# Optimization experiments

Hardware: AMD Instinct MI355X
Metric: run time of the kernel (lower is better)

The kernel has to match this reference:

```python
import jax, jax.numpy as jnp
import numpy as np

N = 50000   # nodes (cells)
E = 800000  # directed edges
D = 512     # input/output feature dim (genes)
H = D // 64 # bottleneck dim = 8
LN_EPS = 1e-5


def setup_inputs() -> dict:
    key = jax.random.key(0)
    ks = jax.random.split(key, 6)
    x = jax.random.normal(ks[0], (N, D), dtype=jnp.float32)
    edge_index = jax.random.randint(ks[1], (2, E), 0, N, dtype=jnp.int64)
    size_factors = jax.random.uniform(ks[2], (N, 1), dtype=jnp.float32) + 0.5
    s1 = float(1.0 / np.sqrt(D))
    W1 = jax.random.uniform(ks[3], (D, H), jnp.float32, -s1, s1)
    b1 = jnp.zeros((H,), jnp.float32)
    gamma = jnp.ones((H,), jnp.float32)
    beta = jnp.zeros((H,), jnp.float32)
    s2 = float(1.0 / np.sqrt(H))
    W2 = jax.random.uniform(ks[4], (H, D), jnp.float32, -s2, s2)
    b2 = jnp.zeros((D,), jnp.float32)
    return {"x": x, "size_factors": size_factors, "W1": W1, "b1": b1,
            "gamma": gamma, "beta": beta, "W2": W2, "b2": b2,
            "edge_index": edge_index}


def _gcn_conv(x, W, b, src, dst, norm):
    # PyG GCNConv: linear transform, then sym-normalized scatter-add aggregation.
    h = x @ W                                   # [N, out]
    msg = h[src] * norm[:, None]                # [E+N, out] gather + scale
    out = jax.ops.segment_sum(msg, dst, num_segments=N)  # scatter-add
    return out + b


def reference(x, size_factors, W1, b1, gamma, beta, W2, b2, edge_index):
    loops = jnp.arange(N, dtype=edge_index.dtype)
    src = jnp.concatenate([edge_index[0], loops])  # add self-loops
    dst = jnp.concatenate([edge_index[1], loops])
    deg = jax.ops.segment_sum(jnp.ones_like(src, dtype=x.dtype), dst,
                              num_segments=N)       # deg >= 1 via self-loops
    dinv = jax.lax.rsqrt(deg)
    norm = dinv[src] * dinv[dst]                    # [E+N]

    h = _gcn_conv(x, W1, b1, src, dst, norm)        # [N, H]
    mu = jnp.mean(h, axis=-1, keepdims=True)
    var = jnp.var(h, axis=-1, keepdims=True)
    h = (h - mu) * jax.lax.rsqrt(var + LN_EPS) * gamma + beta
    h = jax.nn.relu(h)
    # dropout p=0.0 -> identity
    out = jax.nn.relu(_gcn_conv(h, W2, b2, src, dst, norm))  # [N, D]
    return out * size_factors
```

## Files before the change

### kernel.cpp

```cpp
#include <hip/hip_runtime.h>

#define NN 50000
#define EE 800000
#define DD 512
#define HH 8
#define SLOTS 64
#define NBLK 196
#define NTILE (NN/16)
#define EBLK (EE/256)

typedef short bf16x8 __attribute__((ext_vector_type(8)));
typedef float f32x4 __attribute__((ext_vector_type(4)));

union U16 { uint4 u; bf16x8 v; unsigned short h[8]; };

__device__ __forceinline__ unsigned short f2bf(float f) {
    union { float f; unsigned int i; } c; c.f = f;
    unsigned int i = c.i;
    i += 0x7fffu + ((i >> 16) & 1u);
    return (unsigned short)(i >> 16);
}

__global__ void k_fill_ell(const int* __restrict__ src, const int* __restrict__ dst,
                           int* __restrict__ cur, int* __restrict__ slots) {
    int e = blockIdx.x * 256 + threadIdx.x;
    if (e >= EE) return;
    int s = src[e], d = dst[e];
    int pos = atomicAdd(&cur[d], 1);
    if (pos < SLOTS) slots[(size_t)pos * NN + d] = s;
}

__global__ __launch_bounds__(256) void k_gemm1(const float4* __restrict__ x4,
                                               const float* __restrict__ W1,
                                               float* __restrict__ t1) {
    __shared__ unsigned short sbf[16 * 64 * 8];
    for (int i = threadIdx.x; i < 16 * 64 * 8; i += 256) {
        int lane = (i >> 3) & 63, j = i & 7;
        int n = lane & 15;
        int k = (i >> 9) * 32 + ((lane >> 4) * 8) + j;
        sbf[i] = (n < HH) ? f2bf(W1[k * HH + n]) : (unsigned short)0;
    }
    __syncthreads();
    int wave = threadIdx.x >> 6, lane = threadIdx.x & 63;
    int tile = blockIdx.x * 4 + wave;
    if (tile >= NTILE) return;
    int node0 = tile * 16;
    int m = lane & 15, q = lane >> 4;
    const float4* xrow = x4 + (size_t)(node0 + m) * (DD / 4) + q * 2;
    const uint4* bfrag = (const uint4*)sbf;
    f32x4 acc = {0.f, 0.f, 0.f, 0.f};
#pragma unroll
    for (int step = 0; step < 16; ++step) {
        float4 u0 = xrow[step * 8];
        float4 u1 = xrow[step * 8 + 1];
        U16 a, b;
        a.h[0] = f2bf(u0.x); a.h[1] = f2bf(u0.y); a.h[2] = f2bf(u0.z); a.h[3] = f2bf(u0.w);
        a.h[4] = f2bf(u1.x); a.h[5] = f2bf(u1.y); a.h[6] = f2bf(u1.z); a.h[7] = f2bf(u1.w);
        b.u = bfrag[step * 64 + lane];
        acc = __builtin_amdgcn_mfma_f32_16x16x32_bf16(a.v, b.v, acc, 0, 0, 0);
    }
    if (m < HH) {
        int base = (node0 + q * 4) * HH + m;
        t1[base]          = acc[0];
        t1[base + HH]     = acc[1];
        t1[base + 2 * HH] = acc[2];
        t1[base + 3 * HH] = acc[3];
    }
}

__global__ void k_agg1(const float4* __restrict__ t1v, const int* __restrict__ cur,
                       const int* __restrict__ slots,
                       const float* __restrict__ b1,
                       const float* __restrict__ gma,
                       const float* __restrict__ bta,
                       float4* __restrict__ h2v) {
    int n = blockIdx.x * 256 + threadIdx.x;
    if (n >= NN) return;
    int deg = cur[n]; if (deg > SLOTS) deg = SLOTS;
    float dv = rsqrtf((float)cur[n] + 1.0f);
    float4 p0 = t1v[2 * n], p1 = t1v[2 * n + 1];
    float a0 = p0.x * dv, a1 = p0.y * dv, a2 = p0.z * dv, a3 = p0.w * dv;
    float a4 = p1.x * dv, a5 = p1.y * dv, a6 = p1.z * dv, a7 = p1.w * dv;
    for (int i = 0; i < deg; ++i) {
        int s = slots[(size_t)i * NN + n];
        float ws = rsqrtf((float)cur[s] + 1.0f);
        float4 q0 = t1v[2 * s], q1 = t1v[2 * s + 1];
        a0 += q0.x * ws; a1 += q0.y * ws; a2 += q0.z * ws; a3 += q0.w * ws;
        a4 += q1.x * ws; a5 += q1.y * ws; a6 += q1.z * ws; a7 += q1.w * ws;
    }
    a0 = a0 * dv + b1[0]; a1 = a1 * dv + b1[1]; a2 = a2 * dv + b1[2]; a3 = a3 * dv + b1[3];
    a4 = a4 * dv + b1[4]; a5 = a5 * dv + b1[5]; a6 = a6 * dv + b1[6]; a7 = a7 * dv + b1[7];
    float mu = (a0 + a1 + a2 + a3 + a4 + a5 + a6 + a7) * 0.125f;
    float d0 = a0 - mu, d1 = a1 - mu, d2 = a2 - mu, d3 = a3 - mu;
    float d4 = a4 - mu, d5 = a5 - mu, d6 = a6 - mu, d7 = a7 - mu;
    float var = (d0*d0 + d1*d1 + d2*d2 + d3*d3 + d4*d4 + d5*d5 + d6*d6 + d7*d7) * 0.125f;
    float rs = rsqrtf(var + 1e-5f);
    float r0 = fmaxf(d0 * rs * gma[0] + bta[0], 0.f);
    float r1 = fmaxf(d1 * rs * gma[1] + bta[1], 0.f);
    float r2 = fmaxf(d2 * rs * gma[2] + bta[2], 0.f);
    float r3 = fmaxf(d3 * rs * gma[3] + bta[3], 0.f);
    float r4 = fmaxf(d4 * rs * gma[4] + bta[4], 0.f);
    float r5 = fmaxf(d5 * rs * gma[5] + bta[5], 0.f);
    float r6 = fmaxf(d6 * rs * gma[6] + bta[6], 0.f);
    float r7 = fmaxf(d7 * rs * gma[7] + bta[7], 0.f);
    h2v[2 * n]     = make_float4(r0, r1, r2, r3);
    h2v[2 * n + 1] = make_float4(r4, r5, r6, r7);
}

__global__ void k_agg2(const float4* __restrict__ h2v, const int* __restrict__ cur,
                       const int* __restrict__ slots, float4* __restrict__ aggv) {
    int n = blockIdx.x * 256 + threadIdx.x;
    if (n >= NN) return;
    int deg = cur[n]; if (deg > SLOTS) deg = SLOTS;
    float dv = rsqrtf((float)cur[n] + 1.0f);
    float4 p0 = h2v[2 * n], p1 = h2v[2 * n + 1];
    float a0 = p0.x * dv, a1 = p0.y * dv, a2 = p0.z * dv, a3 = p0.w * dv;
    float a4 = p1.x * dv, a5 = p1.y * dv, a6 = p1.z * dv, a7 = p1.w * dv;
    for (int i = 0; i < deg; ++i) {
        int s = slots[(size_t)i * NN + n];
        float ws = rsqrtf((float)cur[s] + 1.0f);
        float4 q0 = h2v[2 * s], q1 = h2v[2 * s + 1];
        a0 += q0.x * ws; a1 += q0.y * ws; a2 += q0.z * ws; a3 += q0.w * ws;
        a4 += q1.x * ws; a5 += q1.y * ws; a6 += q1.z * ws; a7 += q1.w * ws;
    }
    aggv[2 * n]     = make_float4(a0 * dv, a1 * dv, a2 * dv, a3 * dv);
    aggv[2 * n + 1] = make_float4(a4 * dv, a5 * dv, a6 * dv, a7 * dv);
}

__global__ __launch_bounds__(256) void k_gemm2(const float4* __restrict__ aggv,
                                               const float* __restrict__ W2,
                                               const float* __restrict__ b2,
                                               const float* __restrict__ sf,
                                               float* __restrict__ out) {
    int c = threadIdx.x & 63;
    int g = threadIdx.x >> 6;
    int d0 = c * 8;
    float w[8][8];
#pragma unroll
    for (int k = 0; k < 8; ++k) {
        float4 u0 = *(const float4*)(W2 + k * DD + d0);
        float4 u1 = *(const float4*)(W2 + k * DD + d0 + 4);
        w[k][0] = u0.x; w[k][1] = u0.y; w[k][2] = u0.z; w[k][3] = u0.w;
        w[k][4] = u1.x; w[k][5] = u1.y; w[k][6] = u1.z; w[k][7] = u1.w;
    }
    float bb[8];
    {
        float4 u0 = *(const float4*)(b2 + d0);
        float4 u1 = *(const float4*)(b2 + d0 + 4);
        bb[0] = u0.x; bb[1] = u0.y; bb[2] = u0.z; bb[3] = u0.w;
        bb[4] = u1.x; bb[5] = u1.y; bb[6] = u1.z; bb[7] = u1.w;
    }
#pragma unroll
    for (int i = 0; i < 8; ++i) {
        int n = blockIdx.x * 32 + i * 4 + g;
        if (n < NN) {
            float4 p0 = aggv[2 * n], p1 = aggv[2 * n + 1];
            float a[8] = {p0.x, p0.y, p0.z, p0.w, p1.x, p1.y, p1.z, p1.w};
            float s = sf[n];
            float acc[8];
#pragma unroll
            for (int j = 0; j < 8; ++j) acc[j] = bb[j];
#pragma unroll
            for (int k = 0; k < 8; ++k)
#pragma unroll
                for (int j = 0; j < 8; ++j) acc[j] += a[k] * w[k][j];
            float4 o0 = make_float4(fmaxf(acc[0], 0.f) * s, fmaxf(acc[1], 0.f) * s,
                                    fmaxf(acc[2], 0.f) * s, fmaxf(acc[3], 0.f) * s);
            float4 o1 = make_float4(fmaxf(acc[4], 0.f) * s, fmaxf(acc[5], 0.f) * s,
                                    fmaxf(acc[6], 0.f) * s, fmaxf(acc[7], 0.f) * s);
            float4* op = (float4*)(out + (size_t)n * DD + d0);
            op[0] = o0;
            op[1] = o1;
        }
    }
}

extern "C" void kernel_launch(void* const* d_in, const int* in_sizes, int n_in,
                              void* d_out, int out_size, void* d_ws, size_t ws_size,
                              hipStream_t stream) {
    (void)in_sizes; (void)n_in; (void)out_size; (void)ws_size;
    const float* x   = (const float*)d_in[0];
    const float* sf  = (const float*)d_in[1];
    const float* W1  = (const float*)d_in[2];
    const float* b1  = (const float*)d_in[3];
    const float* gma = (const float*)d_in[4];
    const float* bta = (const float*)d_in[5];
    const float* W2  = (const float*)d_in[6];
    const float* b2  = (const float*)d_in[7];
    const int* eidx  = (const int*)d_in[8];
    float* out = (float*)d_out;

    char* ws = (char*)d_ws;
    int*   cur   = (int*)(ws + 0);
    int*   slots = (int*)(ws + (1 << 20));
    float* t1    = (float*)(ws + 15 * (1 << 20));
    float* h2    = (float*)(ws + 17 * (1 << 20));
    float* agg2  = (float*)(ws + 19 * (1 << 20));

    hipMemsetAsync(cur, 0, NN * sizeof(int), stream);
    k_fill_ell<<<EBLK, 256, 0, stream>>>(eidx, eidx + EE, cur, slots);
    k_gemm1<<<(NTILE + 3) / 4, 256, 0, stream>>>((const float4*)x, W1, t1);
    k_agg1<<<NBLK, 256, 0, stream>>>((const float4*)t1, cur, slots,
                                     b1, gma, bta, (float4*)h2);
    k_agg2<<<NBLK, 256, 0, stream>>>((const float4*)h2, cur, slots,
                                     (float4*)agg2);
    k_gemm2<<<(NN + 31) / 32, 256, 0, stream>>>((const float4*)agg2, W2, b2, sf, out);
}
```

Measured before the change: 303.6 us.

## Fuse ELL fill with GEMM1, fuse agg2 with GEMM2, parallelize aggregation per feature

Merges the edge-to-ELL fill and the first GEMM into one launch by giving each its own range of block indices. The second aggregation is fused into the output GEMM through shared memory, which removes the agg2 intermediate buffer and one launch. Both aggregations now use 8 threads per node, one per feature, instead of one thread per node. This is meant to raise parallelism and occupancy on the latency-bound gathers, and LayerNorm is computed with shuffles across those 8 threads. In exchange each gathered row is read with more, smaller loads, and the gather loop is unrolled by two with a ballot-based exit.

```diff
diff --git a/kernel.cpp b/kernel.cpp
--- a/kernel.cpp
+++ b/kernel.cpp
@@ -5,9 +5,10 @@
 #define DD 512
 #define HH 8
 #define SLOTS 64
-#define NBLK 196
-#define NTILE (NN/16)
-#define EBLK (EE/256)
+#define GBLK 782
+#define EBLK 3125
+#define NTILE 3125
+#define AGBLK 1563
 
 typedef short bf16x8 __attribute__((ext_vector_type(8)));
 typedef float f32x4 __attribute__((ext_vector_type(4)));
@@ -21,18 +22,21 @@
     return (unsigned short)(i >> 16);
 }
 
-__global__ void k_fill_ell(const int* __restrict__ src, const int* __restrict__ dst,
-                           int* __restrict__ cur, int* __restrict__ slots) {
-    int e = blockIdx.x * 256 + threadIdx.x;
-    if (e >= EE) return;
-    int s = src[e], d = dst[e];
-    int pos = atomicAdd(&cur[d], 1);
-    if (pos < SLOTS) slots[(size_t)pos * NN + d] = s;
-}
-
-__global__ __launch_bounds__(256) void k_gemm1(const float4* __restrict__ x4,
-                                               const float* __restrict__ W1,
-                                               float* __restrict__ t1) {
+__global__ __launch_bounds__(256) void k_fill_gemm1(const int* __restrict__ eidx,
+                                                    const float4* __restrict__ x4,
+                                                    const float* __restrict__ W1,
+                                                    int* __restrict__ cur,
+                                                    int* __restrict__ slots,
+                                                    float* __restrict__ t1) {
+    if (blockIdx.x >= GBLK) {
+        int e = (blockIdx.x - GBLK) * 256 + threadIdx.x;
+        if (e < EE) {
+            int s = eidx[e], d = eidx[EE + e];
+            int pos = atomicAdd(&cur[d], 1);
+            if (pos < SLOTS) slots[(size_t)pos * NN + d] = s;
+        }
+        return;
+    }
     __shared__ unsigned short sbf[16 * 64 * 8];
     for (int i = threadIdx.x; i < 16 * 64 * 8; i += 256) {
         int lane = (i >> 3) & 63, j = i & 7;
@@ -68,73 +72,54 @@
     }
 }
 
-__global__ void k_agg1(const float4* __restrict__ t1v, const int* __restrict__ cur,
-                       const int* __restrict__ slots,
-                       const float* __restrict__ b1,
-                       const float* __restrict__ gma,
-                       const float* __restrict__ bta,
-                       float4* __restrict__ h2v) {
-    int n = blockIdx.x * 256 + threadIdx.x;
+__global__ __launch_bounds__(256) void k_agg1(const float* __restrict__ t1,
+                                              const int* __restrict__ cur,
+                                              const int* __restrict__ slots,
+                                              const float* __restrict__ b1,
+                                              const float* __restrict__ gma,
+                                              const float* __restrict__ bta,
+                                              float* __restrict__ h2) {
+    int gid = blockIdx.x * 256 + threadIdx.x;
+    int n = gid >> 3, f = gid & 7;
     if (n >= NN) return;
-    int deg = cur[n]; if (deg > SLOTS) deg = SLOTS;
-    float dv = rsqrtf((float)cur[n] + 1.0f);
-    float4 p0 = t1v[2 * n], p1 = t1v[2 * n + 1];
-    float a0 = p0.x * dv, a1 = p0.y * dv, a2 = p0.z * dv, a3 = p0.w * dv;
-    float a4 = p1.x * dv, a5 = p1.y * dv, a6 = p1.z * dv, a7 = p1.w * dv;
-    for (int i = 0; i < deg; ++i) {
-        int s = slots[(size_t)i * NN + n];
-        float ws = rsqrtf((float)cur[s] + 1.0f);
-        float4 q0 = t1v[2 * s], q1 = t1v[2 * s + 1];
-        a0 += q0.x * ws; a1 += q0.y * ws; a2 += q0.z * ws; a3 += q0.w * ws;
-        a4 += q1.x * ws; a5 += q1.y * ws; a6 += q1.z * ws; a7 += q1.w * ws;
-    }
-    a0 = a0 * dv + b1[0]; a1 = a1 * dv + b1[1]; a2 = a2 * dv + b1[2]; a3 = a3 * dv + b1[3];
-    a4 = a4 * dv + b1[4]; a5 = a5 * dv + b1[5]; a6 = a6 * dv + b1[6]; a7 = a7 * dv + b1[7];
-    float mu = (a0 + a1 + a2 + a3 + a4 + a5 + a6 + a7) * 0.125f;
-    float d0 = a0 - mu, d1 = a1 - mu, d2 = a2 - mu, d3 = a3 - mu;
-    float d4 = a4 - mu, d5 = a5 - mu, d6 = a6 - mu, d7 = a7 - mu;
-    float var = (d0*d0 + d1*d1 + d2*d2 + d3*d3 + d4*d4 + d5*d5 + d6*d6 + d7*d7) * 0.125f;
+    int degr = cur[n];
+    int deg = degr > SLOTS ? SLOTS : degr;
+    float dv = rsqrtf((float)degr + 1.0f);
+    float acc = t1[(size_t)n * HH + f] * dv;
+    int i = 0;
+    while (__ballot(i < deg)) {
+        int  s0r = slots[(size_t)i * NN + n];
+        int  s1r = slots[(size_t)(i + 1) * NN + n];
+        bool v0 = i < deg, v1 = (i + 1) < deg;
+        int  s0 = v0 ? s0r : 0, s1 = v1 ? s1r : 0;
+        float w0 = v0 ? rsqrtf((float)cur[s0] + 1.0f) : 0.f;
+        float w1 = v1 ? rsqrtf((float)cur[s1] + 1.0f) : 0.f;
+        acc += t1[(size_t)s0 * HH + f] * w0;
+        acc += t1[(size_t)s1 * HH + f] * w1;
+        i += 2;
+    }
+    acc = acc * dv + b1[f];
+    float s = acc;
+    s += __shfl_xor(s, 1); s += __shfl_xor(s, 2); s += __shfl_xor(s, 4);
+    float mu = s * 0.125f;
+    float dx = acc - mu;
+    float sq = dx * dx;
+    sq += __shfl_xor(sq, 1); sq += __shfl_xor(sq, 2); sq += __shfl_xor(sq, 4);
+    float var = sq * 0.125f;
     float rs = rsqrtf(var + 1e-5f);
-    float r0 = fmaxf(d0 * rs * gma[0] + bta[0], 0.f);
-    float r1 = fmaxf(d1 * rs * gma[1] + bta[1], 0.f);
-    float r2 = fmaxf(d2 * rs * gma[2] + bta[2], 0.f);
-    float r3 = fmaxf(d3 * rs * gma[3] + bta[3], 0.f);
-    float r4 = fmaxf(d4 * rs * gma[4] + bta[4], 0.f);
-    float r5 = fmaxf(d5 * rs * gma[5] + bta[5], 0.f);
-    float r6 = fmaxf(d6 * rs * gma[6] + bta[6], 0.f);
-    float r7 = fmaxf(d7 * rs * gma[7] + bta[7], 0.f);
-    h2v[2 * n]     = make_float4(r0, r1, r2, r3);
-    h2v[2 * n + 1] = make_float4(r4, r5, r6, r7);
-}
-
-__global__ void k_agg2(const float4* __restrict__ h2v, const int* __restrict__ cur,
-                       const int* __restrict__ slots, float4* __restrict__ aggv) {
-    int n = blockIdx.x * 256 + threadIdx.x;
-    if (n >= NN) return;
-    int deg = cur[n]; if (deg > SLOTS) deg = SLOTS;
-    float dv = rsqrtf((float)cur[n] + 1.0f);
-    float4 p0 = h2v[2 * n], p1 = h2v[2 * n + 1];
-    float a0 = p0.x * dv, a1 = p0.y * dv, a2 = p0.z * dv, a3 = p0.w * dv;
-    float a4 = p1.x * dv, a5 = p1.y * dv, a6 = p1.z * dv, a7 = p1.w * dv;
-    for (int i = 0; i < deg; ++i) {
-        int s = slots[(size_t)i * NN + n];
-        float ws = rsqrtf((float)cur[s] + 1.0f);
-        float4 q0 = h2v[2 * s], q1 = h2v[2 * s + 1];
-        a0 += q0.x * ws; a1 += q0.y * ws; a2 += q0.z * ws; a3 += q0.w * ws;
-        a4 += q1.x * ws; a5 += q1.y * ws; a6 += q1.z * ws; a7 += q1.w * ws;
-    }
-    aggv[2 * n]     = make_float4(a0 * dv, a1 * dv, a2 * dv, a3 * dv);
-    aggv[2 * n + 1] = make_float4(a4 * dv, a5 * dv, a6 * dv, a7 * dv);
-}
-
-__global__ __launch_bounds__(256) void k_gemm2(const float4* __restrict__ aggv,
-                                               const float* __restrict__ W2,
-                                               const float* __restrict__ b2,
-                                               const float* __restrict__ sf,
-                                               float* __restrict__ out) {
-    int c = threadIdx.x & 63;
-    int g = threadIdx.x >> 6;
-    int d0 = c * 8;
+    h2[(size_t)n * HH + f] = fmaxf(dx * rs * gma[f] + bta[f], 0.f);
+}
+
+__global__ __launch_bounds__(256) void k_agg2_gemm2(const float* __restrict__ h2,
+                                                    const int* __restrict__ cur,
+                                                    const int* __restrict__ slots,
+                                                    const float* __restrict__ W2,
+                                                    const float* __restrict__ b2,
+                                                    const float* __restrict__ sf,
+                                                    float* __restrict__ out) {
+    __shared__ float sA[32 * 8];
+    int tid = threadIdx.x;
+    int c = tid & 63, g = tid >> 6, d0 = c * 8;
     float w[8][8];
 #pragma unroll
     for (int k = 0; k < 8; ++k) {
@@ -150,13 +135,37 @@
         bb[0] = u0.x; bb[1] = u0.y; bb[2] = u0.z; bb[3] = u0.w;
         bb[4] = u1.x; bb[5] = u1.y; bb[6] = u1.z; bb[7] = u1.w;
     }
+    int nl = tid >> 3, f = tid & 7;
+    int n = blockIdx.x * 32 + nl;
+    if (n < NN) {
+        int degr = cur[n];
+        int deg = degr > SLOTS ? SLOTS : degr;
+        float dv = rsqrtf((float)degr + 1.0f);
+        float acc = h2[(size_t)n * HH + f] * dv;
+        int i = 0;
+        while (__ballot(i < deg)) {
+            int  s0r = slots[(size_t)i * NN + n];
+            int  s1r = slots[(size_t)(i + 1) * NN + n];
+            bool v0 = i < deg, v1 = (i + 1) < deg;
+            int  s0 = v0 ? s0r : 0, s1 = v1 ? s1r : 0;
+            float w0 = v0 ? rsqrtf((float)cur[s0] + 1.0f) : 0.f;
+            float w1 = v1 ? rsqrtf((float)cur[s1] + 1.0f) : 0.f;
+            acc += h2[(size_t)s0 * HH + f] * w0;
+            acc += h2[(size_t)s1 * HH + f] * w1;
+            i += 2;
+        }
+        sA[nl * 8 + f] = acc * dv;
+    }
+    __syncthreads();
 #pragma unroll
     for (int i = 0; i < 8; ++i) {
-        int n = blockIdx.x * 32 + i * 4 + g;
-        if (n < NN) {
-            float4 p0 = aggv[2 * n], p1 = aggv[2 * n + 1];
-            float a[8] = {p0.x, p0.y, p0.z, p0.w, p1.x, p1.y, p1.z, p1.w};
-            float s = sf[n];
+        int row = i * 4 + g;
+        int n2 = blockIdx.x * 32 + row;
+        if (n2 < NN) {
+            float a[8];
+#pragma unroll
+            for (int j = 0; j < 8; ++j) a[j] = sA[row * 8 + j];
+            float s = sf[n2];
             float acc[8];
 #pragma unroll
             for (int j = 0; j < 8; ++j) acc[j] = bb[j];
@@ -168,7 +177,7 @@
                                     fmaxf(acc[2], 0.f) * s, fmaxf(acc[3], 0.f) * s);
             float4 o1 = make_float4(fmaxf(acc[4], 0.f) * s, fmaxf(acc[5], 0.f) * s,
                                     fmaxf(acc[6], 0.f) * s, fmaxf(acc[7], 0.f) * s);
-            float4* op = (float4*)(out + (size_t)n * DD + d0);
+            float4* op = (float4*)(out + (size_t)n2 * DD + d0);
             op[0] = o0;
             op[1] = o1;
         }
@@ -193,16 +202,12 @@
     char* ws = (char*)d_ws;
     int*   cur   = (int*)(ws + 0);
     int*   slots = (int*)(ws + (1 << 20));
-    float* t1    = (float*)(ws + 15 * (1 << 20));
-    float* h2    = (float*)(ws + 17 * (1 << 20));
-    float* agg2  = (float*)(ws + 19 * (1 << 20));
+    float* t1    = (float*)(ws + 16 * (1 << 20));
+    float* h2    = (float*)(ws + 18 * (1 << 20));
 
     hipMemsetAsync(cur, 0, NN * sizeof(int), stream);
-    k_fill_ell<<<EBLK, 256, 0, stream>>>(eidx, eidx + EE, cur, slots);
-    k_gemm1<<<(NTILE + 3) / 4, 256, 0, stream>>>((const float4*)x, W1, t1);
-    k_agg1<<<NBLK, 256, 0, stream>>>((const float4*)t1, cur, slots,
-                                     b1, gma, bta, (float4*)h2);
-    k_agg2<<<NBLK, 256, 0, stream>>>((const float4*)h2, cur, slots,
-                                     (float4*)agg2);
-    k_gemm2<<<(NN + 31) / 32, 256, 0, stream>>>((const float4*)agg2, W2, b2, sf, out);
-}
+    k_fill_gemm1<<<GBLK + EBLK, 256, 0, stream>>>(eidx, (const float4*)x, W1,
+                                                  cur, slots, t1);
+    k_agg1<<<AGBLK, 256, 0, stream>>>(t1, cur, slots, b1, gma, bta, h2);
+    k_agg2_gemm2<<<AGBLK, 256, 0, stream>>>(h2, cur, slots, W2, b2, sf, out);
+}
```

After: 297.8 us. No clear change (-1.9%).
